# Kernel optimization log

Hardware: AMD Instinct MI355X
Metric: run time of the kernel (lower is better)

## Reference

```python
import jax, jax.numpy as jnp
import numpy as np
import math

B, M, N = 4, 1024, 70
D, H, L = 256, 8, 4
DFF = 4 * D
DK = D // H
NFREQ = D // 4  # num_freqs_per_scale with 2 length scales


def _ln(x, w, b, eps=1e-5):
    mu = jnp.mean(x, -1, keepdims=True)
    var = jnp.mean((x - mu) ** 2, -1, keepdims=True)
    return (x - mu) / jnp.sqrt(var + eps) * w + b


def setup_inputs() -> dict:
    key = jax.random.key(0)
    ks = iter(jax.random.split(key, 64))
    nk = lambda: next(ks)
    W = lambda *s: jax.random.normal(nk(), s, jnp.float32) * 0.02
    scales = np.logspace(np.log10(0.1), np.log10(3.0), 2)
    fW = jnp.concatenate([jax.random.normal(nk(), (NFREQ, 3), jnp.float32) / float(s) for s in scales], axis=0)
    fb = jax.random.uniform(nk(), (2 * NFREQ,), jnp.float32) * 2.0 * math.pi
    return {
        "X": jax.random.normal(nk(), (B, M, N), jnp.float32),
        "mask": jnp.ones((B, M, M), jnp.int32),
        "fourier_W": fW, "fourier_b": fb,
        "char_W": W(N - 6, D), "char_b": jnp.zeros((D,)),
        "Wq": W(L, D, D), "bq": jnp.zeros((L, D)),
        "Wk": W(L, D, D), "bk": jnp.zeros((L, D)),
        "Wv": W(L, D, D), "bv": jnp.zeros((L, D)),
        "Wo": W(L, D, D), "bo": jnp.zeros((L, D)),
        "ln1_w": jnp.ones((L, D)), "ln1_b": jnp.zeros((L, D)),
        "ln2_w": jnp.ones((L, D)), "ln2_b": jnp.zeros((L, D)),
        "lnf_w": jnp.ones((D,)), "lnf_b": jnp.zeros((D,)),
        "mlp_uw": W(L, D, DFF), "mlp_ub": jnp.zeros((L, DFF)),
        "mlp_dw": W(L, DFF, D), "mlp_db": jnp.zeros((L, D)),
        "final_w": W(D, N - 6), "final_b": jnp.zeros((N - 6,)),
        "sn_w": jnp.ones((H,)), "sn_b": jnp.zeros((H,)),
        "sfp_w": W(H, 1), "sfp_b": jnp.zeros((1,)),
    }


def reference(X, mask, fourier_W, fourier_b, char_W, char_b,
              Wq, bq, Wk, bk, Wv, bv, Wo, bo,
              ln1_w, ln1_b, ln2_w, ln2_b, lnf_w, lnf_b,
              mlp_uw, mlp_ub, mlp_dw, mlp_db,
              final_w, final_b, sn_w, sn_b, sfp_w, sfp_b):
    b, m, _ = X.shape
    positions = X[:, :, :3]
    # Fourier random features positional embedding (B, m, D)
    proj = positions @ fourier_W.T + fourier_b
    pe = jnp.concatenate([jnp.cos(proj), jnp.sin(proj)], -1) * math.sqrt(2.0 / NFREQ)
    x = X[:, :, 6:] @ char_W + char_b + pe

    scores = None
    for i in range(L):
        xn = _ln(x, ln1_w[i], ln1_b[i])
        q = (xn @ Wq[i] + bq[i]).reshape(b, m, H, DK)
        k = (xn @ Wk[i] + bk[i]).reshape(b, m, H, DK)
        v = (xn @ Wv[i] + bv[i]).reshape(b, m, H, DK)
        scores = jnp.einsum('bqhd,bkhd->bhqk', q, k) / math.sqrt(DK)  # raw (pre-mask) scores, as returned by torch module
        masked = jnp.where(mask[:, None, :, :] == 0, -jnp.inf, scores)
        w = jax.nn.softmax(masked, axis=-1)
        att = jnp.einsum('bhqk,bkhd->bqhd', w, v).reshape(b, m, D)
        x = x + att @ Wo[i] + bo[i]
        xn2 = _ln(x, ln2_w[i], ln2_b[i])
        x = x + jax.nn.gelu(xn2 @ mlp_uw[i] + mlp_ub[i], approximate=False) @ mlp_dw[i] + mlp_db[i]

    x = _ln(x, lnf_w, lnf_b) @ final_w + final_b  # (B, m, n-6)
    s = jnp.transpose(scores, (0, 2, 3, 1))       # (B, q, k, H)
    s = _ln(s, sn_w, sn_b)
    s = (s @ sfp_w + sfp_b)[..., 0]               # (B, m, m)
    s = (jnp.swapaxes(s, 1, 2) + s) / 2.0
    return (x, s)
```

## Files before the change

kernel.cpp:

```cpp
#include <hip/hip_runtime.h>
#include <hip/hip_bf16.h>
#include <math.h>

#define B_ 4
#define M_ 1024
#define NIN 70
#define D_ 256
#define H_ 8
#define L_ 4
#define DFF_ 1024
#define BM_TOT 4096

typedef __hip_bfloat16 bf16;
typedef short short8 __attribute__((ext_vector_type(8)));
typedef float f32x4 __attribute__((ext_vector_type(4)));

__global__ __launch_bounds__(256) void wconv_all(
    const float* __restrict__ Wq, const float* __restrict__ Wk, const float* __restrict__ Wv,
    const float* __restrict__ Wo, const float* __restrict__ uw, const float* __restrict__ dw,
    const float* __restrict__ finw,
    bf16* __restrict__ wqkvt, bf16* __restrict__ wot, bf16* __restrict__ uwt,
    bf16* __restrict__ dwt, bf16* __restrict__ fwt)
{
  __shared__ float T[64][65];
  int idx = blockIdx.x;
  const float* src; bf16* dst; int K, N, k0, n0, rbase, S;
  if (idx < 192) {
    int m = idx >> 6; int r = idx & 63; int l = r >> 4; int tt = r & 15;
    int kt = tt >> 2, nt = tt & 3;
    src = (m == 0 ? Wq : (m == 1 ? Wk : Wv)) + (size_t)l * 65536;
    K = 256; N = 256; k0 = kt * 64; n0 = nt * 64;
    dst = wqkvt + (size_t)l * 196608; rbase = m * 256 + nt * 64; S = 256;
  } else if (idx < 256) {
    int r = idx - 192; int l = r >> 4; int tt = r & 15; int kt = tt >> 2, nt = tt & 3;
    src = Wo + (size_t)l * 65536; K = 256; N = 256; k0 = kt * 64; n0 = nt * 64;
    dst = wot + (size_t)l * 65536; rbase = nt * 64; S = 256;
  } else if (idx < 512) {
    int r = idx - 256; int l = r >> 6; int tt = r & 63; int kt = tt >> 4, nt = tt & 15;
    src = uw + (size_t)l * 262144; K = 256; N = 1024; k0 = kt * 64; n0 = nt * 64;
    dst = uwt + (size_t)l * 262144; rbase = nt * 64; S = 256;
  } else if (idx < 768) {
    int r = idx - 512; int l = r >> 6; int tt = r & 63; int kt = tt >> 2, nt = tt & 3;
    src = dw + (size_t)l * 262144; K = 1024; N = 256; k0 = kt * 64; n0 = nt * 64;
    dst = dwt + (size_t)l * 262144; rbase = nt * 64; S = 1024;
  } else {
    int kt = idx - 768;
    src = finw; K = 256; N = 64; k0 = kt * 64; n0 = 0;
    dst = fwt; rbase = 0; S = 256;
  }
  int t = threadIdx.x;
  int kl = t >> 2, ns = (t & 3) * 16;
  #pragma unroll
  for (int i = 0; i < 16; i += 4)
    *(float4*)&T[kl][ns + i] = *(const float4*)&src[(size_t)(k0 + kl) * N + n0 + ns + i];
  __syncthreads();
  int nl = t >> 2, ks = (t & 3) * 16;
  __align__(16) bf16 tmp[16];
  #pragma unroll
  for (int i = 0; i < 16; ++i) tmp[i] = __float2bfloat16(T[ks + i][nl]);
  *(uint4*)&dst[(size_t)(rbase + nl) * S + k0 + ks] = *(uint4*)&tmp[0];
  *(uint4*)&dst[(size_t)(rbase + nl) * S + k0 + ks + 8] = *(uint4*)&tmp[8];
}

__global__ __launch_bounds__(256) void k_embed(const float* __restrict__ X,
    const float* __restrict__ fW, const float* __restrict__ fb,
    const float* __restrict__ cW, const float* __restrict__ cb,
    float* __restrict__ x)
{
  int bm0 = blockIdx.x * 4;
  int d = threadIdx.x;
  __shared__ float xr[4][NIN];
  for (int i = d; i < 4 * NIN; i += 256)
    xr[i / NIN][i % NIN] = X[(size_t)(bm0 + i / NIN) * NIN + i % NIN];
  __syncthreads();
  int f = d & 127;
  float fw0 = fW[f * 3 + 0], fw1 = fW[f * 3 + 1], fw2 = fW[f * 3 + 2], fbv = fb[f];
  float cbv = cb[d];
  float acc[4];
  #pragma unroll
  for (int r = 0; r < 4; ++r) {
    float proj = xr[r][0] * fw0 + xr[r][1] * fw1 + xr[r][2] * fw2 + fbv;
    acc[r] = (d < 128 ? cosf(proj) : sinf(proj)) * 0.17677669529663687f + cbv;
  }
  #pragma unroll 8
  for (int c = 0; c < 64; ++c) {
    float cw = cW[c * D_ + d];
    #pragma unroll
    for (int r = 0; r < 4; ++r) acc[r] += xr[r][6 + c] * cw;
  }
  #pragma unroll
  for (int r = 0; r < 4; ++r)
    x[(size_t)(bm0 + r) * D_ + d] = acc[r];
}

__global__ __launch_bounds__(256) void k_ln(const float* __restrict__ xin,
    const float* __restrict__ w, const float* __restrict__ b, bf16* __restrict__ xout)
{
  int wave = threadIdx.x >> 6;
  int lane = threadIdx.x & 63;
  int row = blockIdx.x * 4 + wave;
  float4 xv = *(const float4*)&xin[row * D_ + lane * 4];
  float s = xv.x + xv.y + xv.z + xv.w;
  float q = xv.x * xv.x + xv.y * xv.y + xv.z * xv.z + xv.w * xv.w;
  #pragma unroll
  for (int off = 32; off; off >>= 1) {
    s += __shfl_xor(s, off, 64);
    q += __shfl_xor(q, off, 64);
  }
  float mu = s * (1.0f / D_);
  float var = q * (1.0f / D_) - mu * mu;
  float rstd = rsqrtf(var + 1e-5f);
  float4 wv = *(const float4*)&w[lane * 4];
  float4 bv = *(const float4*)&b[lane * 4];
  __align__(8) bf16 tmp[4];
  tmp[0] = __float2bfloat16((xv.x - mu) * rstd * wv.x + bv.x);
  tmp[1] = __float2bfloat16((xv.y - mu) * rstd * wv.y + bv.y);
  tmp[2] = __float2bfloat16((xv.z - mu) * rstd * wv.z + bv.z);
  tmp[3] = __float2bfloat16((xv.w - mu) * rstd * wv.w + bv.w);
  *(uint2*)&xout[row * D_ + lane * 4] = *(uint2*)tmp;
}

__global__ __launch_bounds__(256) void mgemm(const bf16* __restrict__ Ab,
    const bf16* __restrict__ Wt, const float* __restrict__ bias,
    const float* __restrict__ Res, float* __restrict__ Cf, bf16* __restrict__ Cb,
    int K, int N, int flags)
{
  __shared__ short As[64][40];
  __shared__ short Bs[64][40];
  int t = threadIdx.x;
  int m0 = blockIdx.y * 64, n0 = blockIdx.x * 64;
  int w = t >> 6, lane = t & 63;
  int srow = t >> 2, sseg = t & 3;
  f32x4 acc[4] = {{0.f,0.f,0.f,0.f},{0.f,0.f,0.f,0.f},{0.f,0.f,0.f,0.f},{0.f,0.f,0.f,0.f}};
  int mf = w * 16 + (lane & 15);
  int kf = (lane >> 4) * 8;
  const bf16* pA = Ab + (size_t)(m0 + srow) * K + sseg * 8;
  const bf16* pB = Wt + (size_t)(n0 + srow) * K + sseg * 8;
  uint4 ra = *(const uint4*)pA;
  uint4 rb = *(const uint4*)pB;
  for (int k0 = 0; k0 < K; k0 += 32) {
    *(uint4*)&As[srow][sseg * 8] = ra;
    *(uint4*)&Bs[srow][sseg * 8] = rb;
    __syncthreads();
    if (k0 + 32 < K) {
      ra = *(const uint4*)(pA + k0 + 32);
      rb = *(const uint4*)(pB + k0 + 32);
    }
    short8 a = *(short8*)&As[mf][kf];
    #pragma unroll
    for (int nt = 0; nt < 4; ++nt) {
      short8 bfr = *(short8*)&Bs[nt * 16 + (lane & 15)][kf];
      acc[nt] = __builtin_amdgcn_mfma_f32_16x16x32_bf16(a, bfr, acc[nt], 0, 0, 0);
    }
    __syncthreads();
  }
  int row0 = m0 + w * 16 + (lane >> 4) * 4;
  #pragma unroll
  for (int nt = 0; nt < 4; ++nt) {
    int col = n0 + nt * 16 + (lane & 15);
    float bs = bias[col];
    #pragma unroll
    for (int r = 0; r < 4; ++r) {
      float v = acc[nt][r] + bs;
      if (flags & 1) v = 0.5f * v * (1.0f + erff(v * 0.70710678118654752f));
      if (flags & 2) v += Res[(size_t)(row0 + r) * N + col];
      if (flags & 8) Cf[(size_t)(row0 + r) * N + col] = v;
      if (flags & 4) Cb[(size_t)(row0 + r) * N + col] = __float2bfloat16(v);
    }
  }
}

__global__ __launch_bounds__(512) void mgemm512(const bf16* __restrict__ Ab,
    const bf16* __restrict__ Wt, const float* __restrict__ bias,
    const float* __restrict__ Res, float* __restrict__ Cf, bf16* __restrict__ Cb,
    int K, int N, int flags)
{
  __shared__ short As[64][40];
  __shared__ short Bs[64][40];
  int t = threadIdx.x;
  int m0 = blockIdx.y * 64, n0 = blockIdx.x * 64;
  int w = t >> 6, lane = t & 63;
  int l16 = lane & 15, quad = lane >> 4;
  int s = t & 255;
  int srow = s >> 2, sseg = s & 3;
  bool isA = (t < 256);
  short (*S)[40] = isA ? As : Bs;
  const bf16* pS = (isA ? Ab + (size_t)(m0 + srow) * K
                        : Wt + (size_t)(n0 + srow) * K) + sseg * 8;
  uint4 ra = *(const uint4*)pS;
  f32x4 acc[2] = {{0.f,0.f,0.f,0.f},{0.f,0.f,0.f,0.f}};
  int mf = (w & 3) * 16 + l16;
  int kf = quad * 8;
  int ntb = (w >> 2) * 2;
  for (int k0 = 0; k0 < K; k0 += 32) {
    *(uint4*)&S[srow][sseg * 8] = ra;
    __syncthreads();
    if (k0 + 32 < K) ra = *(const uint4*)(pS + k0 + 32);
    short8 a = *(short8*)&As[mf][kf];
    #pragma unroll
    for (int i = 0; i < 2; ++i) {
      short8 bfr = *(short8*)&Bs[(ntb + i) * 16 + l16][kf];
      acc[i] = __builtin_amdgcn_mfma_f32_16x16x32_bf16(a, bfr, acc[i], 0, 0, 0);
    }
    __syncthreads();
  }
  int row0 = m0 + (w & 3) * 16 + quad * 4;
  #pragma unroll
  for (int i = 0; i < 2; ++i) {
    int col = n0 + (ntb + i) * 16 + l16;
    float bs = bias[col];
    #pragma unroll
    for (int r = 0; r < 4; ++r) {
      float v = acc[i][r] + bs;
      if (flags & 1) v = 0.5f * v * (1.0f + erff(v * 0.70710678118654752f));
      if (flags & 2) v += Res[(size_t)(row0 + r) * N + col];
      if (flags & 8) Cf[(size_t)(row0 + r) * N + col] = v;
      if (flags & 4) Cb[(size_t)(row0 + r) * N + col] = __float2bfloat16(v);
    }
  }
}

__global__ __launch_bounds__(256) void mgemm_qkv(const bf16* __restrict__ Ab,
    const bf16* __restrict__ Wt, const float* __restrict__ bq,
    const float* __restrict__ bk, const float* __restrict__ bv,
    bf16* __restrict__ qo, bf16* __restrict__ ko, bf16* __restrict__ vo)
{
  __shared__ short As[64][40];
  __shared__ short Bs[64][40];
  int t = threadIdx.x;
  int m0 = blockIdx.y * 64, n0g = blockIdx.x * 64;
  int w = t >> 6, lane = t & 63;
  int srow = t >> 2, sseg = t & 3;
  f32x4 acc[4] = {{0.f,0.f,0.f,0.f},{0.f,0.f,0.f,0.f},{0.f,0.f,0.f,0.f},{0.f,0.f,0.f,0.f}};
  int mf = w * 16 + (lane & 15);
  int kf = (lane >> 4) * 8;
  const bf16* pA = Ab + (size_t)(m0 + srow) * 256 + sseg * 8;
  const bf16* pB = Wt + (size_t)(n0g + srow) * 256 + sseg * 8;
  uint4 ra = *(const uint4*)pA;
  uint4 rb = *(const uint4*)pB;
  for (int k0 = 0; k0 < 256; k0 += 32) {
    *(uint4*)&As[srow][sseg * 8] = ra;
    *(uint4*)&Bs[srow][sseg * 8] = rb;
    __syncthreads();
    if (k0 + 32 < 256) {
      ra = *(const uint4*)(pA + k0 + 32);
      rb = *(const uint4*)(pB + k0 + 32);
    }
    short8 a = *(short8*)&As[mf][kf];
    #pragma unroll
    for (int nt = 0; nt < 4; ++nt) {
      short8 bfr = *(short8*)&Bs[nt * 16 + (lane & 15)][kf];
      acc[nt] = __builtin_amdgcn_mfma_f32_16x16x32_bf16(a, bfr, acc[nt], 0, 0, 0);
    }
    __syncthreads();
  }
  int seg = n0g >> 8;
  const float* bb = (seg == 0 ? bq : (seg == 1 ? bk : bv));
  bf16* dst = (seg == 0 ? qo : (seg == 1 ? ko : vo));
  int row0 = m0 + w * 16 + (lane >> 4) * 4;
  #pragma unroll
  for (int nt = 0; nt < 4; ++nt) {
    int col = (n0g & 255) + nt * 16 + (lane & 15);
    float bs = bb[col];
    #pragma unroll
    for (int r = 0; r < 4; ++r)
      dst[(size_t)(row0 + r) * 256 + col] = __float2bfloat16(acc[nt][r] + bs);
  }
}

__global__ __launch_bounds__(256) void k_flash(const bf16* __restrict__ q,
    const bf16* __restrict__ k, const bf16* __restrict__ v, bf16* __restrict__ o)
{
  int qt = blockIdx.x, h = blockIdx.y, b = blockIdx.z;
  int t = threadIdx.x;
  int w = t >> 6, lane = t & 63;
  int quad = lane >> 4, l16 = lane & 15;
  __shared__ short Ks[64][40];
  __shared__ short Vt[32][76];
  __shared__ short Pl[4][16][72];
  short8 a_q = *(const short8*)&q[((size_t)(b * M_) + qt * 64 + w * 16 + l16) * D_ + h * 32 + quad * 8];
  f32x4 o_acc[2] = {{0.f,0.f,0.f,0.f},{0.f,0.f,0.f,0.f}};
  float l_acc[4] = {0.f, 0.f, 0.f, 0.f};
  int skey = t >> 2, sseg = t & 3;
  const float scale = 0.17677669529663687f;
  for (int kt = 0; kt < 16; ++kt) {
    __syncthreads();
    *(short8*)&Ks[skey][sseg * 8] =
        *(const short8*)&k[((size_t)(b * M_) + kt * 64 + skey) * D_ + h * 32 + sseg * 8];
    short8 vv = *(const short8*)&v[((size_t)(b * M_) + kt * 64 + skey) * D_ + h * 32 + sseg * 8];
    #pragma unroll
    for (int i = 0; i < 8; ++i) Vt[sseg * 8 + i][skey] = vv[i];
    __syncthreads();
    #pragma unroll
    for (int st = 0; st < 4; ++st) {
      short8 bf = *(short8*)&Ks[st * 16 + l16][quad * 8];
      f32x4 s4 = __builtin_amdgcn_mfma_f32_16x16x32_bf16(a_q, bf, (f32x4){0.f,0.f,0.f,0.f}, 0, 0, 0);
      #pragma unroll
      for (int r = 0; r < 4; ++r) {
        float p = __expf(s4[r] * scale);
        l_acc[r] += p;
        bf16 hb = __float2bfloat16(p);
        Pl[w][quad * 4 + r][st * 16 + l16] = *reinterpret_cast<short*>(&hb);
      }
    }
    asm volatile("s_waitcnt lgkmcnt(0)" ::: "memory");
    #pragma unroll
    for (int kh = 0; kh < 2; ++kh) {
      short8 a_p = *(short8*)&Pl[w][l16][kh * 32 + quad * 8];
      #pragma unroll
      for (int nt = 0; nt < 2; ++nt) {
        short8 b_v = *(short8*)&Vt[nt * 16 + l16][kh * 32 + quad * 8];
        o_acc[nt] = __builtin_amdgcn_mfma_f32_16x16x32_bf16(a_p, b_v, o_acc[nt], 0, 0, 0);
      }
    }
  }
  #pragma unroll
  for (int r = 0; r < 4; ++r) {
    float lv = l_acc[r];
    lv += __shfl_xor(lv, 1, 64);
    lv += __shfl_xor(lv, 2, 64);
    lv += __shfl_xor(lv, 4, 64);
    lv += __shfl_xor(lv, 8, 64);
    l_acc[r] = 1.0f / lv;
  }
  #pragma unroll
  for (int nt = 0; nt < 2; ++nt)
    #pragma unroll
    for (int r = 0; r < 4; ++r)
      o[((size_t)(b * M_) + qt * 64 + w * 16 + quad * 4 + r) * D_ + h * 32 + nt * 16 + l16] =
          __float2bfloat16(o_acc[nt][r] * l_acc[r]);
}

__global__ __launch_bounds__(256) void k_shead1(const bf16* __restrict__ q3,
    const bf16* __restrict__ k3, const float* __restrict__ snw, const float* __restrict__ snb,
    const float* __restrict__ sfw, const float* __restrict__ sfb, float* __restrict__ stmp)
{
  int ct = blockIdx.x, rt = blockIdx.y, b = blockIdx.z;
  int t = threadIdx.x;
  int w = t >> 6, lane = t & 63;
  int quad = lane >> 4, l16 = lane & 15;
  const float scale = 0.17677669529663687f;
  float wsn[H_], bsn[H_], wsf[H_];
  #pragma unroll
  for (int h = 0; h < H_; ++h) { wsn[h] = snw[h]; bsn[h] = snb[h]; wsf[h] = sfw[h]; }
  float bias0 = sfb[0];
  short8 aqs[H_];
  #pragma unroll
  for (int h = 0; h < H_; ++h)
    aqs[h] = *(const short8*)&q3[((size_t)(b * M_) + rt * 64 + w * 16 + l16) * D_ + h * 32 + quad * 8];
  #pragma unroll
  for (int cf = 0; cf < 4; ++cf) {
    f32x4 s4[H_];
    #pragma unroll
    for (int h = 0; h < H_; ++h) {
      short8 bk = *(const short8*)&k3[((size_t)(b * M_) + ct * 64 + cf * 16 + l16) * D_ + h * 32 + quad * 8];
      s4[h] = __builtin_amdgcn_mfma_f32_16x16x32_bf16(aqs[h], bk, (f32x4){0.f,0.f,0.f,0.f}, 0, 0, 0);
    }
    #pragma unroll
    for (int r = 0; r < 4; ++r) {
      float d8[H_], ssum = 0.f, ssq = 0.f;
      #pragma unroll
      for (int h = 0; h < H_; ++h) {
        float s = s4[h][r] * scale;
        d8[h] = s; ssum += s; ssq += s * s;
      }
      float mu = ssum * 0.125f;
      float var = ssq * 0.125f - mu * mu;
      float rstd = rsqrtf(var + 1e-5f);
      float val = bias0;
      #pragma unroll
      for (int h = 0; h < H_; ++h)
        val += ((d8[h] - mu) * rstd * wsn[h] + bsn[h]) * wsf[h];
      stmp[((size_t)(b * M_) + rt * 64 + w * 16 + quad * 4 + r) * M_ + ct * 64 + cf * 16 + l16] = val;
    }
  }
}

__global__ __launch_bounds__(256) void k_sym(const float* __restrict__ stmp,
    float* __restrict__ outs)
{
  int ct = blockIdx.x, rt = blockIdx.y, b = blockIdx.z;
  __shared__ float Tb[64][68];
  int t = threadIdx.x;
  int row = t >> 2, seg = (t & 3) * 16;
  const float* srcB = stmp + ((size_t)(b * M_) + ct * 64 + row) * M_ + rt * 64 + seg;
  #pragma unroll
  for (int i = 0; i < 16; i += 4) {
    float4 v = *(const float4*)(srcB + i);
    Tb[seg + i + 0][row] = v.x;
    Tb[seg + i + 1][row] = v.y;
    Tb[seg + i + 2][row] = v.z;
    Tb[seg + i + 3][row] = v.w;
  }
  __syncthreads();
  const float* srcA = stmp + ((size_t)(b * M_) + rt * 64 + row) * M_ + ct * 64 + seg;
  float* dst = outs + ((size_t)(b * M_) + rt * 64 + row) * M_ + ct * 64 + seg;
  #pragma unroll
  for (int i = 0; i < 16; i += 4) {
    float4 a = *(const float4*)(srcA + i);
    float4 tv = *(const float4*)&Tb[row][seg + i];
    float4 o;
    o.x = 0.5f * (a.x + tv.x);
    o.y = 0.5f * (a.y + tv.y);
    o.z = 0.5f * (a.z + tv.z);
    o.w = 0.5f * (a.w + tv.w);
    *(float4*)(dst + i) = o;
  }
}

extern "C" void kernel_launch(void* const* d_in, const int* in_sizes, int n_in,
                              void* d_out, int out_size, void* d_ws, size_t ws_size,
                              hipStream_t stream)
{
  const float* X    = (const float*)d_in[0];
  const float* fW   = (const float*)d_in[2];
  const float* fb   = (const float*)d_in[3];
  const float* cW   = (const float*)d_in[4];
  const float* cb   = (const float*)d_in[5];
  const float* Wq   = (const float*)d_in[6];
  const float* bq   = (const float*)d_in[7];
  const float* Wk   = (const float*)d_in[8];
  const float* bk   = (const float*)d_in[9];
  const float* Wv   = (const float*)d_in[10];
  const float* bv   = (const float*)d_in[11];
  const float* Wo   = (const float*)d_in[12];
  const float* bo   = (const float*)d_in[13];
  const float* ln1w = (const float*)d_in[14];
  const float* ln1b = (const float*)d_in[15];
  const float* ln2w = (const float*)d_in[16];
  const float* ln2b = (const float*)d_in[17];
  const float* lnfw = (const float*)d_in[18];
  const float* lnfb = (const float*)d_in[19];
  const float* uw   = (const float*)d_in[20];
  const float* ub   = (const float*)d_in[21];
  const float* dw   = (const float*)d_in[22];
  const float* db   = (const float*)d_in[23];
  const float* finw = (const float*)d_in[24];
  const float* finb = (const float*)d_in[25];
  const float* snw  = (const float*)d_in[26];
  const float* snb  = (const float*)d_in[27];
  const float* sfw  = (const float*)d_in[28];
  const float* sfb  = (const float*)d_in[29];

  char* base = (char*)d_ws;
  const size_t MiB = 1024 * 1024;
  bf16* q_b   = (bf16*)(base + 0 * MiB);
  bf16* k_b   = (bf16*)(base + 2 * MiB);
  bf16* wqkvt = (bf16*)(base + 4 * MiB);
  bf16* wot   = (bf16*)(base + 5 * MiB + 512 * 1024);
  bf16* uwt   = (bf16*)(base + 6 * MiB);
  bf16* dwt   = (bf16*)(base + 8 * MiB);
  bf16* fwt   = (bf16*)(base + 10 * MiB);
  float* x    = (float*)(base + 10 * MiB + 512 * 1024);
  char* SR    = base + 14 * MiB + 512 * 1024;
  bf16* xn_b  = (bf16*)(SR + 0 * MiB);
  bf16* v_b   = (bf16*)(SR + 2 * MiB);
  bf16* att_b = (bf16*)(SR + 4 * MiB);
  bf16* h1_b  = (bf16*)(SR + 6 * MiB);
  float* stmp = (float*)(base + 32 * MiB);
  float* outx = (float*)d_out;
  float* outs = outx + (size_t)BM_TOT * 64;

  dim3 blk(256);
  dim3 blk512(512);
  wconv_all<<<dim3(772), blk, 0, stream>>>(Wq, Wk, Wv, Wo, uw, dw, finw,
                                           wqkvt, wot, uwt, dwt, fwt);
  k_embed<<<dim3(BM_TOT / 4), blk, 0, stream>>>(X, fW, fb, cW, cb, x);
  for (int l = 0; l < L_; ++l) {
    k_ln<<<dim3(BM_TOT / 4), blk, 0, stream>>>(x, ln1w + l * D_, ln1b + l * D_, xn_b);
    mgemm_qkv<<<dim3(12, 64), blk, 0, stream>>>(xn_b, wqkvt + (size_t)l * 196608,
                                                bq + l * D_, bk + l * D_, bv + l * D_,
                                                q_b, k_b, v_b);
    k_flash<<<dim3(16, H_, B_), blk, 0, stream>>>(q_b, k_b, v_b, att_b);
    mgemm512<<<dim3(4, 64), blk512, 0, stream>>>(att_b, wot + (size_t)l * 65536, bo + l * D_,
                                                 x, x, nullptr, 256, 256, 2 | 8);
    k_ln<<<dim3(BM_TOT / 4), blk, 0, stream>>>(x, ln2w + l * D_, ln2b + l * D_, xn_b);
    mgemm<<<dim3(16, 64), blk, 0, stream>>>(xn_b, uwt + (size_t)l * 262144, ub + l * DFF_,
                                            nullptr, nullptr, h1_b, 256, 1024, 1 | 4);
    mgemm512<<<dim3(4, 64), blk512, 0, stream>>>(h1_b, dwt + (size_t)l * 262144, db + l * D_,
                                                 x, x, nullptr, 1024, 256, 2 | 8);
  }
  k_ln<<<dim3(BM_TOT / 4), blk, 0, stream>>>(x, lnfw, lnfb, xn_b);
  mgemm512<<<dim3(1, 64), blk512, 0, stream>>>(xn_b, fwt, finb, nullptr, outx, nullptr, 256, 64, 8);
  k_shead1<<<dim3(16, 16, B_), blk, 0, stream>>>(q_b, k_b, snw, snb, sfw, sfb, stmp);
  k_sym<<<dim3(16, 16, B_), blk, 0, stream>>>(stmp, outs);
}
```

Measured before the change: 462.1 us.

## Fuse LayerNorm into GEMM prologues using row statistics from producer epilogues

```diff
diff --git a/kernel.cpp b/kernel.cpp
--- a/kernel.cpp
+++ b/kernel.cpp
@@ -15,15 +15,69 @@
 typedef short short8 __attribute__((ext_vector_type(8)));
 typedef float f32x4 __attribute__((ext_vector_type(4)));
 
-__global__ __launch_bounds__(256) void wconv_all(
+
+__global__ __launch_bounds__(256) void wconv_embed(
     const float* __restrict__ Wq, const float* __restrict__ Wk, const float* __restrict__ Wv,
     const float* __restrict__ Wo, const float* __restrict__ uw, const float* __restrict__ dw,
     const float* __restrict__ finw,
     bf16* __restrict__ wqkvt, bf16* __restrict__ wot, bf16* __restrict__ uwt,
-    bf16* __restrict__ dwt, bf16* __restrict__ fwt)
+    bf16* __restrict__ dwt, bf16* __restrict__ fwt,
+    const float* __restrict__ X, const float* __restrict__ fW, const float* __restrict__ fb,
+    const float* __restrict__ cW, const float* __restrict__ cb,
+    float* __restrict__ x, float* __restrict__ psum)
 {
   __shared__ float T[64][65];
+  __shared__ float xr[4][NIN];
+  __shared__ float red[4][4][2];
   int idx = blockIdx.x;
+  int t = threadIdx.x;
+  if (idx >= 772) {
+    int bm0 = (idx - 772) * 4;
+    int d = t;
+    for (int i = d; i < 4 * NIN; i += 256)
+      xr[i / NIN][i % NIN] = X[(size_t)(bm0 + i / NIN) * NIN + i % NIN];
+    __syncthreads();
+    int f = d & 127;
+    float fw0 = fW[f * 3 + 0], fw1 = fW[f * 3 + 1], fw2 = fW[f * 3 + 2], fbv = fb[f];
+    float cbv = cb[d];
+    float acc[4];
+    #pragma unroll
+    for (int r = 0; r < 4; ++r) {
+      float proj = xr[r][0] * fw0 + xr[r][1] * fw1 + xr[r][2] * fw2 + fbv;
+      acc[r] = (d < 128 ? cosf(proj) : sinf(proj)) * 0.17677669529663687f + cbv;
+    }
+    #pragma unroll 8
+    for (int c = 0; c < 64; ++c) {
+      float cw = cW[c * D_ + d];
+      #pragma unroll
+      for (int r = 0; r < 4; ++r) acc[r] += xr[r][6 + c] * cw;
+    }
+    #pragma unroll
+    for (int r = 0; r < 4; ++r)
+      x[(size_t)(bm0 + r) * D_ + d] = acc[r];
+    int wave = d >> 6, lane = d & 63;
+    #pragma unroll
+    for (int r = 0; r < 4; ++r) {
+      float s = acc[r], qq = acc[r] * acc[r];
+      #pragma unroll
+      for (int off = 32; off; off >>= 1) {
+        s += __shfl_xor(s, off, 64);
+        qq += __shfl_xor(qq, off, 64);
+      }
+      if (lane == 0) { red[wave][r][0] = s; red[wave][r][1] = qq; }
+    }
+    __syncthreads();
+    if (t < 8) {
+      int r = t >> 1, c = t & 1;
+      float v = red[0][r][c] + red[1][r][c] + red[2][r][c] + red[3][r][c];
+      psum[((size_t)0 * BM_TOT + bm0 + r) * 2 + c] = v;
+    } else if (t < 64) {
+      int i = t - 8;
+      int slot = 1 + i / 8; int rr = (i & 7) >> 1; int c = i & 1;
+      psum[((size_t)slot * BM_TOT + bm0 + rr) * 2 + c] = 0.f;
+    }
+    return;
+  }
   const float* src; bf16* dst; int K, N, k0, n0, rbase, S;
   if (idx < 192) {
     int m = idx >> 6; int r = idx & 63; int l = r >> 4; int tt = r & 15;
@@ -48,7 +102,6 @@
     src = finw; K = 256; N = 64; k0 = kt * 64; n0 = 0;
     dst = fwt; rbase = 0; S = 256;
   }
-  int t = threadIdx.x;
   int kl = t >> 2, ns = (t & 3) * 16;
   #pragma unroll
   for (int i = 0; i < 16; i += 4)
@@ -62,118 +115,10 @@
   *(uint4*)&dst[(size_t)(rbase + nl) * S + k0 + ks + 8] = *(uint4*)&tmp[8];
 }
 
-__global__ __launch_bounds__(256) void k_embed(const float* __restrict__ X,
-    const float* __restrict__ fW, const float* __restrict__ fb,
-    const float* __restrict__ cW, const float* __restrict__ cb,
-    float* __restrict__ x)
-{
-  int bm0 = blockIdx.x * 4;
-  int d = threadIdx.x;
-  __shared__ float xr[4][NIN];
-  for (int i = d; i < 4 * NIN; i += 256)
-    xr[i / NIN][i % NIN] = X[(size_t)(bm0 + i / NIN) * NIN + i % NIN];
-  __syncthreads();
-  int f = d & 127;
-  float fw0 = fW[f * 3 + 0], fw1 = fW[f * 3 + 1], fw2 = fW[f * 3 + 2], fbv = fb[f];
-  float cbv = cb[d];
-  float acc[4];
-  #pragma unroll
-  for (int r = 0; r < 4; ++r) {
-    float proj = xr[r][0] * fw0 + xr[r][1] * fw1 + xr[r][2] * fw2 + fbv;
-    acc[r] = (d < 128 ? cosf(proj) : sinf(proj)) * 0.17677669529663687f + cbv;
-  }
-  #pragma unroll 8
-  for (int c = 0; c < 64; ++c) {
-    float cw = cW[c * D_ + d];
-    #pragma unroll
-    for (int r = 0; r < 4; ++r) acc[r] += xr[r][6 + c] * cw;
-  }
-  #pragma unroll
-  for (int r = 0; r < 4; ++r)
-    x[(size_t)(bm0 + r) * D_ + d] = acc[r];
-}
-
-__global__ __launch_bounds__(256) void k_ln(const float* __restrict__ xin,
-    const float* __restrict__ w, const float* __restrict__ b, bf16* __restrict__ xout)
-{
-  int wave = threadIdx.x >> 6;
-  int lane = threadIdx.x & 63;
-  int row = blockIdx.x * 4 + wave;
-  float4 xv = *(const float4*)&xin[row * D_ + lane * 4];
-  float s = xv.x + xv.y + xv.z + xv.w;
-  float q = xv.x * xv.x + xv.y * xv.y + xv.z * xv.z + xv.w * xv.w;
-  #pragma unroll
-  for (int off = 32; off; off >>= 1) {
-    s += __shfl_xor(s, off, 64);
-    q += __shfl_xor(q, off, 64);
-  }
-  float mu = s * (1.0f / D_);
-  float var = q * (1.0f / D_) - mu * mu;
-  float rstd = rsqrtf(var + 1e-5f);
-  float4 wv = *(const float4*)&w[lane * 4];
-  float4 bv = *(const float4*)&b[lane * 4];
-  __align__(8) bf16 tmp[4];
-  tmp[0] = __float2bfloat16((xv.x - mu) * rstd * wv.x + bv.x);
-  tmp[1] = __float2bfloat16((xv.y - mu) * rstd * wv.y + bv.y);
-  tmp[2] = __float2bfloat16((xv.z - mu) * rstd * wv.z + bv.z);
-  tmp[3] = __float2bfloat16((xv.w - mu) * rstd * wv.w + bv.w);
-  *(uint2*)&xout[row * D_ + lane * 4] = *(uint2*)tmp;
-}
-
-__global__ __launch_bounds__(256) void mgemm(const bf16* __restrict__ Ab,
-    const bf16* __restrict__ Wt, const float* __restrict__ bias,
-    const float* __restrict__ Res, float* __restrict__ Cf, bf16* __restrict__ Cb,
-    int K, int N, int flags)
-{
-  __shared__ short As[64][40];
-  __shared__ short Bs[64][40];
-  int t = threadIdx.x;
-  int m0 = blockIdx.y * 64, n0 = blockIdx.x * 64;
-  int w = t >> 6, lane = t & 63;
-  int srow = t >> 2, sseg = t & 3;
-  f32x4 acc[4] = {{0.f,0.f,0.f,0.f},{0.f,0.f,0.f,0.f},{0.f,0.f,0.f,0.f},{0.f,0.f,0.f,0.f}};
-  int mf = w * 16 + (lane & 15);
-  int kf = (lane >> 4) * 8;
-  const bf16* pA = Ab + (size_t)(m0 + srow) * K + sseg * 8;
-  const bf16* pB = Wt + (size_t)(n0 + srow) * K + sseg * 8;
-  uint4 ra = *(const uint4*)pA;
-  uint4 rb = *(const uint4*)pB;
-  for (int k0 = 0; k0 < K; k0 += 32) {
-    *(uint4*)&As[srow][sseg * 8] = ra;
-    *(uint4*)&Bs[srow][sseg * 8] = rb;
-    __syncthreads();
-    if (k0 + 32 < K) {
-      ra = *(const uint4*)(pA + k0 + 32);
-      rb = *(const uint4*)(pB + k0 + 32);
-    }
-    short8 a = *(short8*)&As[mf][kf];
-    #pragma unroll
-    for (int nt = 0; nt < 4; ++nt) {
-      short8 bfr = *(short8*)&Bs[nt * 16 + (lane & 15)][kf];
-      acc[nt] = __builtin_amdgcn_mfma_f32_16x16x32_bf16(a, bfr, acc[nt], 0, 0, 0);
-    }
-    __syncthreads();
-  }
-  int row0 = m0 + w * 16 + (lane >> 4) * 4;
-  #pragma unroll
-  for (int nt = 0; nt < 4; ++nt) {
-    int col = n0 + nt * 16 + (lane & 15);
-    float bs = bias[col];
-    #pragma unroll
-    for (int r = 0; r < 4; ++r) {
-      float v = acc[nt][r] + bs;
-      if (flags & 1) v = 0.5f * v * (1.0f + erff(v * 0.70710678118654752f));
-      if (flags & 2) v += Res[(size_t)(row0 + r) * N + col];
-      if (flags & 8) Cf[(size_t)(row0 + r) * N + col] = v;
-      if (flags & 4) Cb[(size_t)(row0 + r) * N + col] = __float2bfloat16(v);
-    }
-  }
-}
-
 __global__ __launch_bounds__(512) void mgemm512(const bf16* __restrict__ Ab,
     const bf16* __restrict__ Wt, const float* __restrict__ bias,
     const float* __restrict__ Res, float* __restrict__ Cf, bf16* __restrict__ Cb,
-    int K, int N, int flags)
+    float* __restrict__ psum, int K, int N, int flags)
 {
   __shared__ short As[64][40];
   __shared__ short Bs[64][40];
@@ -205,6 +150,7 @@
     __syncthreads();
   }
   int row0 = m0 + (w & 3) * 16 + quad * 4;
+  float vv[2][4];
   #pragma unroll
   for (int i = 0; i < 2; ++i) {
     int col = n0 + (ntb + i) * 16 + l16;
@@ -214,15 +160,34 @@
       float v = acc[i][r] + bs;
       if (flags & 1) v = 0.5f * v * (1.0f + erff(v * 0.70710678118654752f));
       if (flags & 2) v += Res[(size_t)(row0 + r) * N + col];
+      vv[i][r] = v;
       if (flags & 8) Cf[(size_t)(row0 + r) * N + col] = v;
       if (flags & 4) Cb[(size_t)(row0 + r) * N + col] = __float2bfloat16(v);
     }
   }
-}
-
-__global__ __launch_bounds__(256) void mgemm_qkv(const bf16* __restrict__ Ab,
-    const bf16* __restrict__ Wt, const float* __restrict__ bq,
-    const float* __restrict__ bk, const float* __restrict__ bv,
+  if (flags & 16) {
+    int slot = blockIdx.x * 2 + (w >> 2);
+    #pragma unroll
+    for (int r = 0; r < 4; ++r) {
+      float sv = vv[0][r] + vv[1][r];
+      float sq = vv[0][r] * vv[0][r] + vv[1][r] * vv[1][r];
+      #pragma unroll
+      for (int off = 1; off < 16; off <<= 1) {
+        sv += __shfl_xor(sv, off, 64);
+        sq += __shfl_xor(sq, off, 64);
+      }
+      if (l16 == 0) {
+        psum[((size_t)slot * BM_TOT + row0 + r) * 2 + 0] = sv;
+        psum[((size_t)slot * BM_TOT + row0 + r) * 2 + 1] = sq;
+      }
+    }
+  }
+}
+
+__global__ __launch_bounds__(256) void mgemm_qkv_ln(const float* __restrict__ xf,
+    const float* __restrict__ psum, const bf16* __restrict__ Wt,
+    const float* __restrict__ lw, const float* __restrict__ lb,
+    const float* __restrict__ bq, const float* __restrict__ bk, const float* __restrict__ bv,
     bf16* __restrict__ qo, bf16* __restrict__ ko, bf16* __restrict__ vo)
 {
   __shared__ short As[64][40];
@@ -231,19 +196,45 @@
   int m0 = blockIdx.y * 64, n0g = blockIdx.x * 64;
   int w = t >> 6, lane = t & 63;
   int srow = t >> 2, sseg = t & 3;
+  int gr = m0 + srow;
+  float sv = 0.f, sq = 0.f;
+  #pragma unroll
+  for (int i = 0; i < 8; ++i) {
+    float2 p = *(const float2*)&psum[((size_t)i * BM_TOT + gr) * 2];
+    sv += p.x; sq += p.y;
+  }
+  float mu = sv * (1.0f / D_);
+  float rstd = rsqrtf(sq * (1.0f / D_) - mu * mu + 1e-5f);
+  int c0 = sseg * 8;
+  const float* pX = xf + (size_t)gr * D_;
+  const bf16* pB = Wt + (size_t)(n0g + srow) * 256 + c0;
+  float4 xa = *(const float4*)(pX + c0);
+  float4 xb = *(const float4*)(pX + c0 + 4);
+  uint4 rb = *(const uint4*)pB;
   f32x4 acc[4] = {{0.f,0.f,0.f,0.f},{0.f,0.f,0.f,0.f},{0.f,0.f,0.f,0.f},{0.f,0.f,0.f,0.f}};
   int mf = w * 16 + (lane & 15);
   int kf = (lane >> 4) * 8;
-  const bf16* pA = Ab + (size_t)(m0 + srow) * 256 + sseg * 8;
-  const bf16* pB = Wt + (size_t)(n0g + srow) * 256 + sseg * 8;
-  uint4 ra = *(const uint4*)pA;
-  uint4 rb = *(const uint4*)pB;
   for (int k0 = 0; k0 < 256; k0 += 32) {
-    *(uint4*)&As[srow][sseg * 8] = ra;
-    *(uint4*)&Bs[srow][sseg * 8] = rb;
+    int c = k0 + c0;
+    float4 wa = *(const float4*)(lw + c);
+    float4 wb = *(const float4*)(lw + c + 4);
+    float4 ba = *(const float4*)(lb + c);
+    float4 bb = *(const float4*)(lb + c + 4);
+    __align__(16) bf16 tb[8];
+    tb[0] = __float2bfloat16((xa.x - mu) * rstd * wa.x + ba.x);
+    tb[1] = __float2bfloat16((xa.y - mu) * rstd * wa.y + ba.y);
+    tb[2] = __float2bfloat16((xa.z - mu) * rstd * wa.z + ba.z);
+    tb[3] = __float2bfloat16((xa.w - mu) * rstd * wa.w + ba.w);
+    tb[4] = __float2bfloat16((xb.x - mu) * rstd * wb.x + bb.x);
+    tb[5] = __float2bfloat16((xb.y - mu) * rstd * wb.y + bb.y);
+    tb[6] = __float2bfloat16((xb.z - mu) * rstd * wb.z + bb.z);
+    tb[7] = __float2bfloat16((xb.w - mu) * rstd * wb.w + bb.w);
+    *(uint4*)&As[srow][c0] = *(uint4*)tb;
+    *(uint4*)&Bs[srow][c0] = rb;
     __syncthreads();
     if (k0 + 32 < 256) {
-      ra = *(const uint4*)(pA + k0 + 32);
+      xa = *(const float4*)(pX + c + 32);
+      xb = *(const float4*)(pX + c + 36);
       rb = *(const uint4*)(pB + k0 + 32);
     }
     short8 a = *(short8*)&As[mf][kf];
@@ -255,16 +246,92 @@
     __syncthreads();
   }
   int seg = n0g >> 8;
-  const float* bb = (seg == 0 ? bq : (seg == 1 ? bk : bv));
+  const float* bbv = (seg == 0 ? bq : (seg == 1 ? bk : bv));
   bf16* dst = (seg == 0 ? qo : (seg == 1 ? ko : vo));
   int row0 = m0 + w * 16 + (lane >> 4) * 4;
   #pragma unroll
   for (int nt = 0; nt < 4; ++nt) {
     int col = (n0g & 255) + nt * 16 + (lane & 15);
-    float bs = bb[col];
+    float bs = bbv[col];
     #pragma unroll
     for (int r = 0; r < 4; ++r)
       dst[(size_t)(row0 + r) * 256 + col] = __float2bfloat16(acc[nt][r] + bs);
+  }
+}
+
+__global__ __launch_bounds__(256) void mgemmA_ln(const float* __restrict__ xf,
+    const float* __restrict__ psum, const bf16* __restrict__ Wt,
+    const float* __restrict__ lw, const float* __restrict__ lb,
+    const float* __restrict__ bias, float* __restrict__ Cf, bf16* __restrict__ Cb,
+    int N, int flags)
+{
+  __shared__ short As[64][40];
+  __shared__ short Bs[64][40];
+  int t = threadIdx.x;
+  int m0 = blockIdx.y * 64, n0 = blockIdx.x * 64;
+  int w = t >> 6, lane = t & 63;
+  int srow = t >> 2, sseg = t & 3;
+  int gr = m0 + srow;
+  float sv = 0.f, sq = 0.f;
+  #pragma unroll
+  for (int i = 0; i < 8; ++i) {
+    float2 p = *(const float2*)&psum[((size_t)i * BM_TOT + gr) * 2];
+    sv += p.x; sq += p.y;
+  }
+  float mu = sv * (1.0f / D_);
+  float rstd = rsqrtf(sq * (1.0f / D_) - mu * mu + 1e-5f);
+  int c0 = sseg * 8;
+  const float* pX = xf + (size_t)gr * D_;
+  const bf16* pB = Wt + (size_t)(n0 + srow) * 256 + c0;
+  float4 xa = *(const float4*)(pX + c0);
+  float4 xb = *(const float4*)(pX + c0 + 4);
+  uint4 rb = *(const uint4*)pB;
+  f32x4 acc[4] = {{0.f,0.f,0.f,0.f},{0.f,0.f,0.f,0.f},{0.f,0.f,0.f,0.f},{0.f,0.f,0.f,0.f}};
+  int mf = w * 16 + (lane & 15);
+  int kf = (lane >> 4) * 8;
+  for (int k0 = 0; k0 < 256; k0 += 32) {
+    int c = k0 + c0;
+    float4 wa = *(const float4*)(lw + c);
+    float4 wb = *(const float4*)(lw + c + 4);
+    float4 ba = *(const float4*)(lb + c);
+    float4 bb = *(const float4*)(lb + c + 4);
+    __align__(16) bf16 tb[8];
+    tb[0] = __float2bfloat16((xa.x - mu) * rstd * wa.x + ba.x);
+    tb[1] = __float2bfloat16((xa.y - mu) * rstd * wa.y + ba.y);
+    tb[2] = __float2bfloat16((xa.z - mu) * rstd * wa.z + ba.z);
+    tb[3] = __float2bfloat16((xa.w - mu) * rstd * wa.w + ba.w);
+    tb[4] = __float2bfloat16((xb.x - mu) * rstd * wb.x + bb.x);
+    tb[5] = __float2bfloat16((xb.y - mu) * rstd * wb.y + bb.y);
+    tb[6] = __float2bfloat16((xb.z - mu) * rstd * wb.z + bb.z);
+    tb[7] = __float2bfloat16((xb.w - mu) * rstd * wb.w + bb.w);
+    *(uint4*)&As[srow][c0] = *(uint4*)tb;
+    *(uint4*)&Bs[srow][c0] = rb;
+    __syncthreads();
+    if (k0 + 32 < 256) {
+      xa = *(const float4*)(pX + c + 32);
+      xb = *(const float4*)(pX + c + 36);
+      rb = *(const uint4*)(pB + k0 + 32);
+    }
+    short8 a = *(short8*)&As[mf][kf];
+    #pragma unroll
+    for (int nt = 0; nt < 4; ++nt) {
+      short8 bfr = *(short8*)&Bs[nt * 16 + (lane & 15)][kf];
+      acc[nt] = __builtin_amdgcn_mfma_f32_16x16x32_bf16(a, bfr, acc[nt], 0, 0, 0);
+    }
+    __syncthreads();
+  }
+  int row0 = m0 + w * 16 + (lane >> 4) * 4;
+  #pragma unroll
+  for (int nt = 0; nt < 4; ++nt) {
+    int col = n0 + nt * 16 + (lane & 15);
+    float bs = bias[col];
+    #pragma unroll
+    for (int r = 0; r < 4; ++r) {
+      float v = acc[nt][r] + bs;
+      if (flags & 1) v = 0.5f * v * (1.0f + erff(v * 0.70710678118654752f));
+      if (flags & 8) Cf[(size_t)(row0 + r) * N + col] = v;
+      if (flags & 4) Cb[(size_t)(row0 + r) * N + col] = __float2bfloat16(v);
+    }
   }
 }
 
@@ -453,35 +520,35 @@
   bf16* fwt   = (bf16*)(base + 10 * MiB);
   float* x    = (float*)(base + 10 * MiB + 512 * 1024);
   char* SR    = base + 14 * MiB + 512 * 1024;
-  bf16* xn_b  = (bf16*)(SR + 0 * MiB);
   bf16* v_b   = (bf16*)(SR + 2 * MiB);
   bf16* att_b = (bf16*)(SR + 4 * MiB);
   bf16* h1_b  = (bf16*)(SR + 6 * MiB);
+  float* psum = (float*)(base + 30 * MiB);
   float* stmp = (float*)(base + 32 * MiB);
   float* outx = (float*)d_out;
   float* outs = outx + (size_t)BM_TOT * 64;
 
   dim3 blk(256);
   dim3 blk512(512);
-  wconv_all<<<dim3(772), blk, 0, stream>>>(Wq, Wk, Wv, Wo, uw, dw, finw,
-                                           wqkvt, wot, uwt, dwt, fwt);
-  k_embed<<<dim3(BM_TOT / 4), blk, 0, stream>>>(X, fW, fb, cW, cb, x);
+  wconv_embed<<<dim3(772 + BM_TOT / 4), blk, 0, stream>>>(
+      Wq, Wk, Wv, Wo, uw, dw, finw, wqkvt, wot, uwt, dwt, fwt,
+      X, fW, fb, cW, cb, x, psum);
   for (int l = 0; l < L_; ++l) {
-    k_ln<<<dim3(BM_TOT / 4), blk, 0, stream>>>(x, ln1w + l * D_, ln1b + l * D_, xn_b);
-    mgemm_qkv<<<dim3(12, 64), blk, 0, stream>>>(xn_b, wqkvt + (size_t)l * 196608,
-                                                bq + l * D_, bk + l * D_, bv + l * D_,
-                                                q_b, k_b, v_b);
+    mgemm_qkv_ln<<<dim3(12, 64), blk, 0, stream>>>(x, psum, wqkvt + (size_t)l * 196608,
+                                                   ln1w + l * D_, ln1b + l * D_,
+                                                   bq + l * D_, bk + l * D_, bv + l * D_,
+                                                   q_b, k_b, v_b);
     k_flash<<<dim3(16, H_, B_), blk, 0, stream>>>(q_b, k_b, v_b, att_b);
     mgemm512<<<dim3(4, 64), blk512, 0, stream>>>(att_b, wot + (size_t)l * 65536, bo + l * D_,
-                                                 x, x, nullptr, 256, 256, 2 | 8);
-    k_ln<<<dim3(BM_TOT / 4), blk, 0, stream>>>(x, ln2w + l * D_, ln2b + l * D_, xn_b);
-    mgemm<<<dim3(16, 64), blk, 0, stream>>>(xn_b, uwt + (size_t)l * 262144, ub + l * DFF_,
-                                            nullptr, nullptr, h1_b, 256, 1024, 1 | 4);
+                                                 x, x, nullptr, psum, 256, 256, 2 | 8 | 16);
+    mgemmA_ln<<<dim3(16, 64), blk, 0, stream>>>(x, psum, uwt + (size_t)l * 262144,
+                                                ln2w + l * D_, ln2b + l * D_,
+                                                ub + l * DFF_, nullptr, h1_b, 1024, 1 | 4);
     mgemm512<<<dim3(4, 64), blk512, 0, stream>>>(h1_b, dwt + (size_t)l * 262144, db + l * D_,
-                                                 x, x, nullptr, 1024, 256, 2 | 8);
-  }
-  k_ln<<<dim3(BM_TOT / 4), blk, 0, stream>>>(x, lnfw, lnfb, xn_b);
-  mgemm512<<<dim3(1, 64), blk512, 0, stream>>>(xn_b, fwt, finb, nullptr, outx, nullptr, 256, 64, 8);
+                                                 x, x, nullptr, psum, 1024, 256, 2 | 8 | 16);
+  }
+  mgemmA_ln<<<dim3(1, 64), blk, 0, stream>>>(x, psum, fwt, lnfw, lnfb,
+                                             finb, outx, nullptr, 64, 8);
   k_shead1<<<dim3(16, 16, B_), blk, 0, stream>>>(q_b, k_b, snw, snb, sfw, sfb, stmp);
   k_sym<<<dim3(16, 16, B_), blk, 0, stream>>>(stmp, outs);
 }
```

New measurement: 476.1 us. +3.0%, slower.

## Fuse score head with symmetrization and prefetch K/V tiles in flash attention

Applied to the files above, without the earlier changes.

```diff
diff --git a/kernel.cpp b/kernel.cpp
--- a/kernel.cpp
+++ b/kernel.cpp
@@ -283,14 +283,19 @@
   float l_acc[4] = {0.f, 0.f, 0.f, 0.f};
   int skey = t >> 2, sseg = t & 3;
   const float scale = 0.17677669529663687f;
+  const bf16* pk = &k[((size_t)(b * M_) + skey) * D_ + h * 32 + sseg * 8];
+  const bf16* pv = &v[((size_t)(b * M_) + skey) * D_ + h * 32 + sseg * 8];
+  short8 rk = *(const short8*)pk;
+  short8 rv = *(const short8*)pv;
   for (int kt = 0; kt < 16; ++kt) {
-    __syncthreads();
-    *(short8*)&Ks[skey][sseg * 8] =
-        *(const short8*)&k[((size_t)(b * M_) + kt * 64 + skey) * D_ + h * 32 + sseg * 8];
-    short8 vv = *(const short8*)&v[((size_t)(b * M_) + kt * 64 + skey) * D_ + h * 32 + sseg * 8];
-    #pragma unroll
-    for (int i = 0; i < 8; ++i) Vt[sseg * 8 + i][skey] = vv[i];
-    __syncthreads();
+    *(short8*)&Ks[skey][sseg * 8] = rk;
+    #pragma unroll
+    for (int i = 0; i < 8; ++i) Vt[sseg * 8 + i][skey] = rv[i];
+    __syncthreads();
+    if (kt < 15) {
+      rk = *(const short8*)(pk + (size_t)(kt + 1) * 64 * D_);
+      rv = *(const short8*)(pv + (size_t)(kt + 1) * 64 * D_);
+    }
     #pragma unroll
     for (int st = 0; st < 4; ++st) {
       short8 bf = *(short8*)&Ks[st * 16 + l16][quad * 8];
@@ -313,6 +318,7 @@
         o_acc[nt] = __builtin_amdgcn_mfma_f32_16x16x32_bf16(a_p, b_v, o_acc[nt], 0, 0, 0);
       }
     }
+    __syncthreads();
   }
   #pragma unroll
   for (int r = 0; r < 4; ++r) {
@@ -331,19 +337,28 @@
           __float2bfloat16(o_acc[nt][r] * l_acc[r]);
 }
 
-__global__ __launch_bounds__(256) void k_shead1(const bf16* __restrict__ q3,
+__global__ __launch_bounds__(512) void k_shead_f(const bf16* __restrict__ q3,
     const bf16* __restrict__ k3, const float* __restrict__ snw, const float* __restrict__ snb,
-    const float* __restrict__ sfw, const float* __restrict__ sfb, float* __restrict__ stmp)
-{
-  int ct = blockIdx.x, rt = blockIdx.y, b = blockIdx.z;
-  int t = threadIdx.x;
-  int w = t >> 6, lane = t & 63;
+    const float* __restrict__ sfw, const float* __restrict__ sfb, float* __restrict__ outs)
+{
+  int p = blockIdx.x, b = blockIdx.z;
+  int it = 0;
+  while ((it + 1) * (it + 2) / 2 <= p) ++it;
+  int jt = p - it * (it + 1) / 2;
+  int t = threadIdx.x;
+  int half = t >> 8;
+  int tl = t & 255;
+  int w = tl >> 6, lane = tl & 63;
   int quad = lane >> 4, l16 = lane & 15;
+  __shared__ float Sa[64][65], Sb[64][65];
   const float scale = 0.17677669529663687f;
   float wsn[H_], bsn[H_], wsf[H_];
   #pragma unroll
   for (int h = 0; h < H_; ++h) { wsn[h] = snw[h]; bsn[h] = snb[h]; wsf[h] = sfw[h]; }
   float bias0 = sfb[0];
+  int rt = half ? jt : it;
+  int ct = half ? it : jt;
+  float (*S)[65] = half ? Sb : Sa;
   short8 aqs[H_];
   #pragma unroll
   for (int h = 0; h < H_; ++h)
@@ -371,40 +386,24 @@
       #pragma unroll
       for (int h = 0; h < H_; ++h)
         val += ((d8[h] - mu) * rstd * wsn[h] + bsn[h]) * wsf[h];
-      stmp[((size_t)(b * M_) + rt * 64 + w * 16 + quad * 4 + r) * M_ + ct * 64 + cf * 16 + l16] = val;
-    }
-  }
-}
-
-__global__ __launch_bounds__(256) void k_sym(const float* __restrict__ stmp,
-    float* __restrict__ outs)
-{
-  int ct = blockIdx.x, rt = blockIdx.y, b = blockIdx.z;
-  __shared__ float Tb[64][68];
-  int t = threadIdx.x;
-  int row = t >> 2, seg = (t & 3) * 16;
-  const float* srcB = stmp + ((size_t)(b * M_) + ct * 64 + row) * M_ + rt * 64 + seg;
-  #pragma unroll
-  for (int i = 0; i < 16; i += 4) {
-    float4 v = *(const float4*)(srcB + i);
-    Tb[seg + i + 0][row] = v.x;
-    Tb[seg + i + 1][row] = v.y;
-    Tb[seg + i + 2][row] = v.z;
-    Tb[seg + i + 3][row] = v.w;
+      S[w * 16 + quad * 4 + r][cf * 16 + l16] = val;
+    }
   }
   __syncthreads();
-  const float* srcA = stmp + ((size_t)(b * M_) + rt * 64 + row) * M_ + ct * 64 + seg;
-  float* dst = outs + ((size_t)(b * M_) + rt * 64 + row) * M_ + ct * 64 + seg;
-  #pragma unroll
-  for (int i = 0; i < 16; i += 4) {
-    float4 a = *(const float4*)(srcA + i);
-    float4 tv = *(const float4*)&Tb[row][seg + i];
-    float4 o;
-    o.x = 0.5f * (a.x + tv.x);
-    o.y = 0.5f * (a.y + tv.y);
-    o.z = 0.5f * (a.z + tv.z);
-    o.w = 0.5f * (a.w + tv.w);
-    *(float4*)(dst + i) = o;
+  bool diag = (it == jt);
+  int i = tl >> 2, j0 = (tl & 3) * 16;
+  if (half == 0) {
+    #pragma unroll
+    for (int jj = 0; jj < 16; ++jj) {
+      int j = j0 + jj;
+      outs[((size_t)(b * M_) + it * 64 + i) * M_ + jt * 64 + j] = 0.5f * (Sa[i][j] + Sb[j][i]);
+    }
+  } else if (!diag) {
+    #pragma unroll
+    for (int ii = 0; ii < 16; ++ii) {
+      int i2 = j0 + ii;
+      outs[((size_t)(b * M_) + jt * 64 + i) * M_ + it * 64 + i2] = 0.5f * (Sb[i][i2] + Sa[i2][i]);
+    }
   }
 }
 
@@ -457,7 +456,6 @@
   bf16* v_b   = (bf16*)(SR + 2 * MiB);
   bf16* att_b = (bf16*)(SR + 4 * MiB);
   bf16* h1_b  = (bf16*)(SR + 6 * MiB);
-  float* stmp = (float*)(base + 32 * MiB);
   float* outx = (float*)d_out;
   float* outs = outx + (size_t)BM_TOT * 64;
 
@@ -482,6 +480,5 @@
   }
   k_ln<<<dim3(BM_TOT / 4), blk, 0, stream>>>(x, lnfw, lnfb, xn_b);
   mgemm512<<<dim3(1, 64), blk512, 0, stream>>>(xn_b, fwt, finb, nullptr, outx, nullptr, 256, 64, 8);
-  k_shead1<<<dim3(16, 16, B_), blk, 0, stream>>>(q_b, k_b, snw, snb, sfw, sfb, stmp);
-  k_sym<<<dim3(16, 16, B_), blk, 0, stream>>>(stmp, outs);
-}
+  k_shead_f<<<dim3(136, 1, B_), blk512, 0, stream>>>(q_b, k_b, snw, snb, sfw, sfb, outs);
+}
```

Result: faster. 437.0 us (-5.4%).
